# Kernel tuning notes

Measured on AMD Instinct MI355X. Metric: run time of the kernel, lower is better.

The kernel has to match this reference:

```python
import jax, jax.numpy as jnp
import numpy as np

N = 50000       # nodes per layer
L = 2           # multiplex layers
F_IN = 128
F_OUT = 32
E_L = 800000    # in-layer edges per layer
NEG_SLOPE = 0.2  # LeakyReLU(0.2)


def _merge_edges(edges_per_layer):
    # offset each layer's edges into the global L*N index space
    parts = [edges_per_layer[i] + i * N for i in range(L)]
    all_edges = jnp.concatenate(parts, axis=1)
    dt = all_edges.dtype
    # self loops on every (layer, node)
    self_loops = jnp.tile(jnp.arange(L * N, dtype=dt)[None, :], (2, 1))
    all_edges = jnp.concatenate([all_edges, self_loops], axis=1)
    # interlayer loops: torch.combinations(arange(L), r=2) + flip([0,1])
    pairs = np.array([(i, j) for i in range(L) for j in range(i + 1, L)], dtype=np.int64)
    pairs = np.concatenate([pairs, pairs[::-1, ::-1]], axis=0)
    all_nodes = np.arange(L * N, dtype=np.int64).reshape(L, N)
    src = all_nodes[pairs[:, 0]].reshape(-1)
    trg = all_nodes[pairs[:, 1]].reshape(-1)
    inter = jnp.asarray(np.stack([src, trg], axis=0)).astype(dt)
    return jnp.concatenate([all_edges, inter], axis=1)  # [2, E_total]


def setup_inputs() -> dict:
    key = jax.random.key(0)
    k1, k2, k3, k4, k5 = jax.random.split(key, 5)
    return {
        "x": jax.random.normal(k1, (1, N, F_IN), dtype=jnp.float32),
        "edge_index0": jax.random.randint(k2, (2, E_L), 0, N, dtype=jnp.int32),
        "edge_index1": jax.random.randint(k3, (2, E_L), 0, N, dtype=jnp.int32),
        "W_proj": jax.random.normal(k4, (L * F_OUT, F_IN), dtype=jnp.float32) * 0.05,
        "W_merge": jax.random.normal(k5, (F_OUT, L * F_OUT), dtype=jnp.float32) * 0.05,
        "bias": jnp.zeros((L, F_OUT), dtype=jnp.float32),
    }


def reference(x, edge_index0, edge_index1, W_proj, W_merge, bias):
    # dropout_prob=0 -> dropout is identity (eval-mode semantics)
    B = x.shape[0]
    edges = _merge_edges([edge_index0, edge_index1])
    src, trg = edges[0], edges[1]
    # degree normalization (naming follows original: in_deg from src, out_deg from trg)
    in_deg = 1.0 / jnp.sqrt(jnp.zeros(L * N, x.dtype).at[src].add(1.0))
    out_deg = 1.0 / jnp.sqrt(jnp.zeros(L * N, x.dtype).at[trg].add(1.0))
    # project F_IN -> L*F_OUT, then split features into L chunks concatenated on node dim
    proj = jnp.einsum('bnf,of->bno', x, W_proj)                 # [B, N, L*F_OUT]
    proj = proj.reshape(B, N, L, F_OUT).transpose(0, 2, 1, 3).reshape(B, L * N, F_OUT)
    proj = proj * out_deg[None, :, None]
    lifted = proj[:, src, :]                                    # [B, E, F_OUT] gather
    agg = jnp.zeros((B, L * N, F_OUT), x.dtype).at[:, trg, :].add(lifted)  # scatter_add
    agg = agg * in_deg[None, :, None]
    out = agg.reshape(B, L, N, F_OUT).transpose(0, 2, 1, 3)     # [B, N, L, F_OUT]
    out = jax.nn.leaky_relu(out + bias, NEG_SLOPE)
    return jnp.einsum('bnk,ok->bno', out.reshape(B, N, L * F_OUT), W_merge)  # [B, N, F_OUT]
```

## Files before the change

kernel.cpp:

```cpp
#include <hip/hip_runtime.h>

#define N_NODES 50000
#define F_IN 128
#define F_OUT 32
#define E_L 800000
#define NEG_SLOPE 0.2f
#define LN 100000
#define NE 1600000
#define BSH 6
#define BNODES 64
#define NB 782
#define CAP 2368
#define PBLOCKS 256
#define PCHUNK 6250
#define CEDGE 13

__global__ __launch_bounds__(512) void partition_kernel(
    const int* __restrict__ e0, const int* __restrict__ e1,
    int* __restrict__ cur_t, int* __restrict__ cur_s,
    int* __restrict__ trgbuf, unsigned char* __restrict__ srcbuf) {
    __shared__ int hist_t[NB], hist_s[NB], res_t[NB], res_s[NB];
    const int t = threadIdx.x, b = blockIdx.x;
    const int l = (b >= PBLOCKS / 2) ? 1 : 0;
    const int* __restrict__ ei = l ? e1 : e0;
    const int ebase = b * PCHUNK - l * E_L;
    for (int i = t; i < NB; i += 512) { hist_t[i] = 0; hist_s[i] = 0; }
    __syncthreads();
    int cu_[CEDGE], ct_[CEDGE], ot_[CEDGE], os_[CEDGE];
    #pragma unroll
    for (int j = 0; j < CEDGE; ++j) {
        const int idx = t + j * 512;
        if (idx < PCHUNK) {
            const int e = ebase + idx;
            const int src = ei[e], trg = ei[E_L + e];
            cu_[j] = src; ct_[j] = trg;
            ot_[j] = atomicAdd(&hist_t[trg >> BSH], 1);
            os_[j] = atomicAdd(&hist_s[src >> BSH], 1);
        } else { cu_[j] = 0; ct_[j] = -1; ot_[j] = 0; os_[j] = 0; }
    }
    __syncthreads();
    for (int i = t; i < NB; i += 512) {
        res_t[i] = hist_t[i] ? atomicAdd(&cur_t[i], hist_t[i]) : 0;
        res_s[i] = hist_s[i] ? atomicAdd(&cur_s[i], hist_s[i]) : 0;
    }
    __syncthreads();
    #pragma unroll
    for (int j = 0; j < CEDGE; ++j) {
        if (ct_[j] >= 0) {
            const int src = cu_[j], trg = ct_[j];
            const int st = res_t[trg >> BSH] + ot_[j];
            const int ss = res_s[src >> BSH] + os_[j];
            if (st < CAP)
                trgbuf[(trg >> BSH) * CAP + st] =
                    (((l << 6) | (trg & 63)) << 17) | (src + l * N_NODES);
            if (ss < CAP)
                srcbuf[(src >> BSH) * CAP + ss] =
                    (unsigned char)((l << 6) | (src & 63));
        }
    }
}

__global__ __launch_bounds__(256) void count_kernel(
    const int* __restrict__ cur_t, const int* __restrict__ cur_s,
    const int* __restrict__ trgbuf, const unsigned char* __restrict__ srcbuf,
    int* __restrict__ cnt_trg, int* __restrict__ cnt_src) {
    __shared__ int ht[128], hs[128];
    const int t = threadIdx.x, b = blockIdx.x;
    if (t < 128) { ht[t] = 0; hs[t] = 0; }
    __syncthreads();
    const int ct = min(cur_t[b], CAP), cs = min(cur_s[b], CAP);
    for (int i = t; i < ct; i += 256)
        atomicAdd(&ht[(trgbuf[b * CAP + i] >> 17) & 127], 1);
    for (int i = t; i < cs; i += 256)
        atomicAdd(&hs[srcbuf[b * CAP + i] & 127], 1);
    __syncthreads();
    if (t < 128) {
        const int l = t >> 6, n = b * BNODES + (t & 63);
        if (n < N_NODES) {
            cnt_trg[l * N_NODES + n] = ht[t];
            cnt_src[l * N_NODES + n] = hs[t];
        }
    }
}

__global__ __launch_bounds__(256) void proj_kernel(
    const float* __restrict__ x, const float* __restrict__ Wp,
    const int* __restrict__ cnt_trg, float* __restrict__ scaled) {
    __shared__ float Wtt[64][132];
    __shared__ float xt[8][F_IN];
    const int t = threadIdx.x;
    for (int i = t; i < 64 * F_IN; i += 256) {
        int o = i >> 7, k = i & 127;
        Wtt[o][k] = Wp[i];
    }
    const int lane = t & 63, w = t >> 6;
    const int ntiles = N_NODES / 8;
    for (int tile = blockIdx.x; tile < ntiles; tile += gridDim.x) {
        const int base = tile * 8;
        __syncthreads();
        ((float4*)&xt[0][0])[t] = ((const float4*)(x + (size_t)base * F_IN))[t];
        __syncthreads();
        const int n0 = w, n1 = w + 4;
        float acc0 = 0.f, acc1 = 0.f;
        #pragma unroll
        for (int k = 0; k < F_IN; k += 4) {
            float4 wv = *(const float4*)&Wtt[lane][k];
            float4 x0 = *(const float4*)&xt[n0][k];
            float4 x1 = *(const float4*)&xt[n1][k];
            acc0 += wv.x * x0.x + wv.y * x0.y + wv.z * x0.z + wv.w * x0.w;
            acc1 += wv.x * x1.x + wv.y * x1.y + wv.z * x1.z + wv.w * x1.w;
        }
        const int l = lane >> 5, f = lane & 31;
        {
            const int v = l * N_NODES + base + n0;
            const float od = 1.0f / sqrtf((float)(cnt_trg[v] + 2));
            scaled[(size_t)v * F_OUT + f] = acc0 * od;
        }
        {
            const int v = l * N_NODES + base + n1;
            const float od = 1.0f / sqrtf((float)(cnt_trg[v] + 2));
            scaled[(size_t)v * F_OUT + f] = acc1 * od;
        }
    }
}

__global__ __launch_bounds__(512) void mega_kernel(
    const int* __restrict__ cur_t, const int* __restrict__ trgbuf,
    const int* __restrict__ cnt_trg, const int* __restrict__ cnt_src,
    const float* __restrict__ scaled, const float* __restrict__ Wm,
    const float* __restrict__ bias, float* __restrict__ out) {
    __shared__ int   colx[CAP];
    __shared__ int   rp[128], rdeg[128], cursor[128], sc[128];
    __shared__ float h[BNODES][64];
    __shared__ float Wt[64][32];
    __shared__ float bs[64];
    const int t = threadIdx.x, b = blockIdx.x;
    for (int i = t; i < 2048; i += 512) Wt[i >> 5][i & 31] = Wm[(i & 31) * 64 + (i >> 5)];
    if (t < 64) bs[t] = bias[t];
    int cnt_r = 0;
    if (t < 128) {
        const int l = t >> 6, n = b * BNODES + (t & 63);
        cnt_r = (n < N_NODES) ? cnt_trg[l * N_NODES + n] : 0;
        rdeg[t] = cnt_r; sc[t] = cnt_r;
    }
    __syncthreads();
    for (int off = 1; off < 128; off <<= 1) {
        int add = (t < 128 && t >= off) ? sc[t - off] : 0;
        __syncthreads();
        if (t < 128) sc[t] += add;
        __syncthreads();
    }
    if (t < 128) { rp[t] = sc[t] - cnt_r; cursor[t] = sc[t] - cnt_r; }
    __syncthreads();
    const int total = min(cur_t[b], CAP);
    for (int i = t; i < total; i += 512) {
        const int p = trgbuf[b * CAP + i];
        const int slot = atomicAdd(&cursor[(p >> 17) & 127], 1);
        colx[slot] = p & 0x1FFFF;
    }
    __syncthreads();
    const int nl = t >> 3, f = (t & 7) * 4;
    const int n = b * BNODES + nl;
    if (n < N_NODES) {
        const int s0 = rp[nl],      d0 = rdeg[nl];
        const int s1 = rp[nl + 64], d1 = rdeg[nl + 64];
        float4 acc0 = make_float4(0.f, 0.f, 0.f, 0.f);
        float4 acc1 = make_float4(0.f, 0.f, 0.f, 0.f);
        const int m = (d0 > d1) ? d0 : d1;
        #pragma unroll 4
        for (int i = 0; i < m; ++i) {
            if (i < d0) {
                const int u = colx[s0 + i];
                const float4 g = *(const float4*)(scaled + (size_t)u * F_OUT + f);
                acc0.x += g.x; acc0.y += g.y; acc0.z += g.z; acc0.w += g.w;
            }
            if (i < d1) {
                const int u = colx[s1 + i];
                const float4 g = *(const float4*)(scaled + (size_t)u * F_OUT + f);
                acc1.x += g.x; acc1.y += g.y; acc1.z += g.z; acc1.w += g.w;
            }
        }
        const int v = n, vp = N_NODES + n;
        const float4 sv = *(const float4*)(scaled + (size_t)v  * F_OUT + f);
        const float4 pv = *(const float4*)(scaled + (size_t)vp * F_OUT + f);
        const float id0 = rsqrtf((float)(cnt_src[v]  + 2));
        const float id1 = rsqrtf((float)(cnt_src[vp] + 2));
        float4 h0, h1;
        h0.x = (acc0.x + sv.x + pv.x) * id0 + bs[f + 0];
        h0.y = (acc0.y + sv.y + pv.y) * id0 + bs[f + 1];
        h0.z = (acc0.z + sv.z + pv.z) * id0 + bs[f + 2];
        h0.w = (acc0.w + sv.w + pv.w) * id0 + bs[f + 3];
        h1.x = (acc1.x + sv.x + pv.x) * id1 + bs[32 + f + 0];
        h1.y = (acc1.y + sv.y + pv.y) * id1 + bs[32 + f + 1];
        h1.z = (acc1.z + sv.z + pv.z) * id1 + bs[32 + f + 2];
        h1.w = (acc1.w + sv.w + pv.w) * id1 + bs[32 + f + 3];
        h0.x = (h0.x >= 0.f) ? h0.x : NEG_SLOPE * h0.x;
        h0.y = (h0.y >= 0.f) ? h0.y : NEG_SLOPE * h0.y;
        h0.z = (h0.z >= 0.f) ? h0.z : NEG_SLOPE * h0.z;
        h0.w = (h0.w >= 0.f) ? h0.w : NEG_SLOPE * h0.w;
        h1.x = (h1.x >= 0.f) ? h1.x : NEG_SLOPE * h1.x;
        h1.y = (h1.y >= 0.f) ? h1.y : NEG_SLOPE * h1.y;
        h1.z = (h1.z >= 0.f) ? h1.z : NEG_SLOPE * h1.z;
        h1.w = (h1.w >= 0.f) ? h1.w : NEG_SLOPE * h1.w;
        *(float4*)&h[nl][f]      = h0;
        *(float4*)&h[nl][32 + f] = h1;
    }
    __syncthreads();
    for (int i = t; i < BNODES * 32; i += 512) {
        const int nl2 = i >> 5, o = i & 31, n2 = b * BNODES + nl2;
        if (n2 < N_NODES) {
            float acc = 0.f;
            #pragma unroll
            for (int k = 0; k < 64; ++k)
                acc += h[nl2][k] * Wt[k][o];
            out[(size_t)n2 * F_OUT + o] = acc;
        }
    }
}

extern "C" void kernel_launch(void* const* d_in, const int* in_sizes, int n_in,
                              void* d_out, int out_size, void* d_ws, size_t ws_size,
                              hipStream_t stream) {
    const float* x    = (const float*)d_in[0];
    const int*   e0   = (const int*)d_in[1];
    const int*   e1   = (const int*)d_in[2];
    const float* Wp   = (const float*)d_in[3];
    const float* Wm   = (const float*)d_in[4];
    const float* bias = (const float*)d_in[5];
    float* out = (float*)d_out;

    float* scaled = (float*)d_ws;
    unsigned char* srcbuf = (unsigned char*)d_ws;
    int* trgbuf  = (int*)((char*)d_ws + (size_t)LN * F_OUT * sizeof(float));
    int* cur_t   = trgbuf + (size_t)NB * CAP;
    int* cur_s   = cur_t + NB;
    int* cnt_trg = cur_s + NB;
    int* cnt_src = cnt_trg + LN;

    hipMemsetAsync(cur_t, 0, 2 * NB * sizeof(int), stream);

    partition_kernel<<<PBLOCKS, 512, 0, stream>>>(e0, e1, cur_t, cur_s,
                                                  trgbuf, srcbuf);
    count_kernel<<<NB, 256, 0, stream>>>(cur_t, cur_s, trgbuf, srcbuf,
                                         cnt_trg, cnt_src);
    proj_kernel<<<1024, 256, 0, stream>>>(x, Wp, cnt_trg, scaled);
    mega_kernel<<<NB, 512, 0, stream>>>(cur_t, trgbuf, cnt_trg, cnt_src,
                                        scaled, Wm, bias, out);
}
```

Baseline: 191.0 us.

## Fuse degree counting into projection and split aggregation blocks into node halves

Merges count_kernel into proj_kernel, so each block counts the target degrees of its 64-node bucket in shared memory and uses them directly for normalization. This removes the cnt_trg global round trip and one launch. mega_kernel now launches twice as many 256-thread blocks, each handling 32 nodes, and recomputes degrees by rescanning the bucket's trgbuf, so the bucket's edges are read once more per half. It also moves srcbuf out of the region it shared with scaled, and caps colx at HCAP, which may drop edges if a half-bucket overflows.

```diff
diff --git a/kernel.cpp b/kernel.cpp
--- a/kernel.cpp
+++ b/kernel.cpp
@@ -11,6 +11,7 @@
 #define BNODES 64
 #define NB 782
 #define CAP 2368
+#define HCAP 1280
 #define PBLOCKS 256
 #define PCHUNK 6250
 #define CEDGE 13
@@ -60,12 +61,17 @@
     }
 }
 
-__global__ __launch_bounds__(256) void count_kernel(
+__global__ __launch_bounds__(256) void proj_kernel(
+    const float* __restrict__ x, const float* __restrict__ Wp,
     const int* __restrict__ cur_t, const int* __restrict__ cur_s,
     const int* __restrict__ trgbuf, const unsigned char* __restrict__ srcbuf,
-    int* __restrict__ cnt_trg, int* __restrict__ cnt_src) {
+    int* __restrict__ cnt_src, float* __restrict__ scaled) {
+    __shared__ float Wtt[64][132];
+    __shared__ float xt[8][F_IN];
     __shared__ int ht[128], hs[128];
     const int t = threadIdx.x, b = blockIdx.x;
+    for (int i = t; i < 64 * F_IN; i += 256)
+        Wtt[i >> 7][i & 127] = Wp[i];
     if (t < 128) { ht[t] = 0; hs[t] = 0; }
     __syncthreads();
     const int ct = min(cur_t[b], CAP), cs = min(cur_s[b], CAP);
@@ -74,96 +80,95 @@
     for (int i = t; i < cs; i += 256)
         atomicAdd(&hs[srcbuf[b * CAP + i] & 127], 1);
     __syncthreads();
+    const int base = b * BNODES;
     if (t < 128) {
-        const int l = t >> 6, n = b * BNODES + (t & 63);
-        if (n < N_NODES) {
-            cnt_trg[l * N_NODES + n] = ht[t];
-            cnt_src[l * N_NODES + n] = hs[t];
-        }
-    }
-}
-
-__global__ __launch_bounds__(256) void proj_kernel(
-    const float* __restrict__ x, const float* __restrict__ Wp,
-    const int* __restrict__ cnt_trg, float* __restrict__ scaled) {
-    __shared__ float Wtt[64][132];
-    __shared__ float xt[8][F_IN];
-    const int t = threadIdx.x;
-    for (int i = t; i < 64 * F_IN; i += 256) {
-        int o = i >> 7, k = i & 127;
-        Wtt[o][k] = Wp[i];
+        const int n = base + (t & 63);
+        if (n < N_NODES) cnt_src[(t >> 6) * N_NODES + n] = hs[t];
     }
     const int lane = t & 63, w = t >> 6;
-    const int ntiles = N_NODES / 8;
-    for (int tile = blockIdx.x; tile < ntiles; tile += gridDim.x) {
-        const int base = tile * 8;
-        __syncthreads();
-        ((float4*)&xt[0][0])[t] = ((const float4*)(x + (size_t)base * F_IN))[t];
-        __syncthreads();
-        const int n0 = w, n1 = w + 4;
+    const int l = lane >> 5, f = lane & 31;
+    for (int s = 0; s < 8; ++s) {
+        const int nb0 = base + s * 8;
+        if (nb0 >= N_NODES) break;
+        __syncthreads();
+        {
+            float4 val = make_float4(0.f, 0.f, 0.f, 0.f);
+            if (nb0 + (t >> 5) < N_NODES)
+                val = ((const float4*)(x + (size_t)nb0 * F_IN))[t];
+            ((float4*)&xt[0][0])[t] = val;
+        }
+        __syncthreads();
+        const int i0 = s * 8 + w, i1 = s * 8 + w + 4;
         float acc0 = 0.f, acc1 = 0.f;
         #pragma unroll
         for (int k = 0; k < F_IN; k += 4) {
             float4 wv = *(const float4*)&Wtt[lane][k];
-            float4 x0 = *(const float4*)&xt[n0][k];
-            float4 x1 = *(const float4*)&xt[n1][k];
+            float4 x0 = *(const float4*)&xt[w][k];
+            float4 x1 = *(const float4*)&xt[w + 4][k];
             acc0 += wv.x * x0.x + wv.y * x0.y + wv.z * x0.z + wv.w * x0.w;
             acc1 += wv.x * x1.x + wv.y * x1.y + wv.z * x1.z + wv.w * x1.w;
         }
-        const int l = lane >> 5, f = lane & 31;
-        {
-            const int v = l * N_NODES + base + n0;
-            const float od = 1.0f / sqrtf((float)(cnt_trg[v] + 2));
-            scaled[(size_t)v * F_OUT + f] = acc0 * od;
-        }
-        {
-            const int v = l * N_NODES + base + n1;
-            const float od = 1.0f / sqrtf((float)(cnt_trg[v] + 2));
-            scaled[(size_t)v * F_OUT + f] = acc1 * od;
-        }
-    }
-}
-
-__global__ __launch_bounds__(512) void mega_kernel(
+        const int n0 = base + i0, n1 = base + i1;
+        if (n0 < N_NODES) {
+            const float od = rsqrtf((float)(ht[(l << 6) | i0] + 2));
+            scaled[(size_t)(l * N_NODES + n0) * F_OUT + f] = acc0 * od;
+        }
+        if (n1 < N_NODES) {
+            const float od = rsqrtf((float)(ht[(l << 6) | i1] + 2));
+            scaled[(size_t)(l * N_NODES + n1) * F_OUT + f] = acc1 * od;
+        }
+    }
+}
+
+__global__ __launch_bounds__(256) void mega_kernel(
     const int* __restrict__ cur_t, const int* __restrict__ trgbuf,
-    const int* __restrict__ cnt_trg, const int* __restrict__ cnt_src,
-    const float* __restrict__ scaled, const float* __restrict__ Wm,
-    const float* __restrict__ bias, float* __restrict__ out) {
-    __shared__ int   colx[CAP];
-    __shared__ int   rp[128], rdeg[128], cursor[128], sc[128];
-    __shared__ float h[BNODES][64];
+    const int* __restrict__ cnt_src, const float* __restrict__ scaled,
+    const float* __restrict__ Wm, const float* __restrict__ bias,
+    float* __restrict__ out) {
+    __shared__ int   colx[HCAP];
+    __shared__ int   rdeg[64], rp[64], cursor[64], sc[64];
+    __shared__ float h[32][64];
     __shared__ float Wt[64][32];
     __shared__ float bs[64];
-    const int t = threadIdx.x, b = blockIdx.x;
-    for (int i = t; i < 2048; i += 512) Wt[i >> 5][i & 31] = Wm[(i & 31) * 64 + (i >> 5)];
-    if (t < 64) bs[t] = bias[t];
+    const int t = threadIdx.x, b2 = blockIdx.x;
+    const int b = b2 >> 1, half = b2 & 1;
+    for (int i = t; i < 2048; i += 256)
+        Wt[i >> 5][i & 31] = Wm[(i & 31) * 64 + (i >> 5)];
+    if (t < 64) { bs[t] = bias[t]; rdeg[t] = 0; }
+    __syncthreads();
+    const int total = min(cur_t[b], CAP);
+    const int tb = b * CAP;
+    for (int i = t; i < total; i += 256) {
+        const int rr = (trgbuf[tb + i] >> 17) & 127;
+        if (((rr >> 5) & 1) == half)
+            atomicAdd(&rdeg[((rr >> 6) << 5) | (rr & 31)], 1);
+    }
+    __syncthreads();
     int cnt_r = 0;
-    if (t < 128) {
-        const int l = t >> 6, n = b * BNODES + (t & 63);
-        cnt_r = (n < N_NODES) ? cnt_trg[l * N_NODES + n] : 0;
-        rdeg[t] = cnt_r; sc[t] = cnt_r;
-    }
-    __syncthreads();
-    for (int off = 1; off < 128; off <<= 1) {
-        int add = (t < 128 && t >= off) ? sc[t - off] : 0;
-        __syncthreads();
-        if (t < 128) sc[t] += add;
-        __syncthreads();
-    }
-    if (t < 128) { rp[t] = sc[t] - cnt_r; cursor[t] = sc[t] - cnt_r; }
-    __syncthreads();
-    const int total = min(cur_t[b], CAP);
-    for (int i = t; i < total; i += 512) {
-        const int p = trgbuf[b * CAP + i];
-        const int slot = atomicAdd(&cursor[(p >> 17) & 127], 1);
-        colx[slot] = p & 0x1FFFF;
+    if (t < 64) { cnt_r = rdeg[t]; sc[t] = cnt_r; }
+    __syncthreads();
+    for (int off = 1; off < 64; off <<= 1) {
+        int add = (t < 64 && t >= off) ? sc[t - off] : 0;
+        __syncthreads();
+        if (t < 64) sc[t] += add;
+        __syncthreads();
+    }
+    if (t < 64) { rp[t] = sc[t] - cnt_r; cursor[t] = sc[t] - cnt_r; }
+    __syncthreads();
+    for (int i = t; i < total; i += 256) {
+        const int p = trgbuf[tb + i];
+        const int rr = (p >> 17) & 127;
+        if (((rr >> 5) & 1) == half) {
+            const int slot = atomicAdd(&cursor[((rr >> 6) << 5) | (rr & 31)], 1);
+            if (slot < HCAP) colx[slot] = p & 0x1FFFF;
+        }
     }
     __syncthreads();
     const int nl = t >> 3, f = (t & 7) * 4;
-    const int n = b * BNODES + nl;
+    const int n = b * BNODES + half * 32 + nl;
     if (n < N_NODES) {
         const int s0 = rp[nl],      d0 = rdeg[nl];
-        const int s1 = rp[nl + 64], d1 = rdeg[nl + 64];
+        const int s1 = rp[nl + 32], d1 = rdeg[nl + 32];
         float4 acc0 = make_float4(0.f, 0.f, 0.f, 0.f);
         float4 acc1 = make_float4(0.f, 0.f, 0.f, 0.f);
         const int m = (d0 > d1) ? d0 : d1;
@@ -206,8 +211,9 @@
         *(float4*)&h[nl][32 + f] = h1;
     }
     __syncthreads();
-    for (int i = t; i < BNODES * 32; i += 512) {
-        const int nl2 = i >> 5, o = i & 31, n2 = b * BNODES + nl2;
+    for (int i = t; i < 32 * 32; i += 256) {
+        const int nl2 = i >> 5, o = i & 31;
+        const int n2 = b * BNODES + half * 32 + nl2;
         if (n2 < N_NODES) {
             float acc = 0.f;
             #pragma unroll
@@ -230,20 +236,18 @@
     float* out = (float*)d_out;
 
     float* scaled = (float*)d_ws;
-    unsigned char* srcbuf = (unsigned char*)d_ws;
-    int* trgbuf  = (int*)((char*)d_ws + (size_t)LN * F_OUT * sizeof(float));
-    int* cur_t   = trgbuf + (size_t)NB * CAP;
+    int* trgbuf  = (int*)(scaled + (size_t)LN * F_OUT);
+    unsigned char* srcbuf = (unsigned char*)(trgbuf + (size_t)NB * CAP);
+    int* cur_t   = (int*)(srcbuf + (size_t)NB * CAP);
     int* cur_s   = cur_t + NB;
-    int* cnt_trg = cur_s + NB;
-    int* cnt_src = cnt_trg + LN;
+    int* cnt_src = cur_s + NB;
 
     hipMemsetAsync(cur_t, 0, 2 * NB * sizeof(int), stream);
 
     partition_kernel<<<PBLOCKS, 512, 0, stream>>>(e0, e1, cur_t, cur_s,
                                                   trgbuf, srcbuf);
-    count_kernel<<<NB, 256, 0, stream>>>(cur_t, cur_s, trgbuf, srcbuf,
-                                         cnt_trg, cnt_src);
-    proj_kernel<<<1024, 256, 0, stream>>>(x, Wp, cnt_trg, scaled);
-    mega_kernel<<<NB, 512, 0, stream>>>(cur_t, trgbuf, cnt_trg, cnt_src,
-                                        scaled, Wm, bias, out);
-}
+    proj_kernel<<<NB, 256, 0, stream>>>(x, Wp, cur_t, cur_s, trgbuf, srcbuf,
+                                        cnt_src, scaled);
+    mega_kernel<<<2 * NB, 256, 0, stream>>>(cur_t, trgbuf, cnt_src,
+                                            scaled, Wm, bias, out);
+}
```

After: 246.5 us. 1.29x slower.
